# Kernel optimization log

Measured on AMD Instinct MI355X. Metric: run time of the kernel, lower is better.

Reference implementation:

```python
import jax, jax.numpy as jnp
import numpy as np

EPS = 1e-5

def _bn_bcn(x, g, b):
    # BatchNorm1d on [B, C, N], training mode: stats over (B, N) per channel
    m = x.mean(axis=(0, 2), keepdims=True)
    v = x.var(axis=(0, 2), keepdims=True)
    return g[None, :, None] * (x - m) * jax.lax.rsqrt(v + EPS) + b[None, :, None]

def _bn_bc(x, g, b):
    # BatchNorm1d on [B, C]
    m = x.mean(axis=0)
    v = x.var(axis=0)
    return g * (x - m) * jax.lax.rsqrt(v + EPS) + b

def _symmetric_orthogonalization(x9):
    # x9: [B, 9] -> [B, 3, 3] in SO(3)
    m = x9.reshape(-1, 3, 3)
    u, s, vt = jnp.linalg.svd(m, full_matrices=False)
    det = jnp.linalg.det(jnp.matmul(u, vt))[:, None, None]
    vt = jnp.concatenate([vt[:, :2, :], vt[:, 2:, :] * det], axis=1)
    return jnp.matmul(u, vt)

def setup_inputs() -> dict:
    key = jax.random.key(0)
    ks = jax.random.split(key, 24)
    B, N = 32, 2048
    def lin(k, out_c, in_c):
        return jax.random.normal(k, (out_c, in_c), jnp.float32) / np.sqrt(in_c)
    inp = {}
    inp['x'] = jax.random.normal(ks[0], (B, 3, N), jnp.float32)
    # conv1x1 weights (kernel size 1 -> per-point linear)
    inp['w1'] = lin(ks[1], 64, 3);    inp['b1'] = jnp.zeros((64,), jnp.float32)
    inp['g1'] = jnp.ones((64,), jnp.float32);   inp['be1'] = jnp.zeros((64,), jnp.float32)
    inp['w2'] = lin(ks[2], 128, 64);  inp['b2'] = jnp.zeros((128,), jnp.float32)
    inp['g2'] = jnp.ones((128,), jnp.float32);  inp['be2'] = jnp.zeros((128,), jnp.float32)
    inp['w3'] = lin(ks[3], 1024, 128); inp['b3'] = jnp.zeros((1024,), jnp.float32)
    inp['g3'] = jnp.ones((1024,), jnp.float32); inp['be3'] = jnp.zeros((1024,), jnp.float32)
    inp['wf1'] = lin(ks[4], 512, 1024); inp['bf1'] = jnp.zeros((512,), jnp.float32)
    inp['gf1'] = jnp.ones((512,), jnp.float32); inp['bef1'] = jnp.zeros((512,), jnp.float32)
    inp['wf2'] = lin(ks[5], 256, 512);  inp['bf2'] = jnp.zeros((256,), jnp.float32)
    inp['gf2'] = jnp.ones((256,), jnp.float32); inp['bef2'] = jnp.zeros((256,), jnp.float32)
    inp['wp'] = lin(ks[6], 12, 256);    inp['bp'] = jnp.zeros((12,), jnp.float32)
    return inp

def reference(x, w1, b1, g1, be1, w2, b2, g2, be2, w3, b3, g3, be3,
              wf1, bf1, gf1, bef1, wf2, bf2, gf2, bef2, wp, bp):
    B = x.shape[0]
    h = jax.nn.relu(_bn_bcn(jnp.einsum('bdn,od->bon', x, w1) + b1[None, :, None], g1, be1))
    h = jax.nn.relu(_bn_bcn(jnp.einsum('bdn,od->bon', h, w2) + b2[None, :, None], g2, be2))
    h = _bn_bcn(jnp.einsum('bdn,od->bon', h, w3) + b3[None, :, None], g3, be3)
    h = jnp.max(h, axis=2)                      # global max pool -> [B, 1024]
    h = jax.nn.relu(_bn_bc(h @ wf1.T + bf1, gf1, bef1))
    h = jax.nn.relu(_bn_bc(h @ wf2.T + bf2, gf2, bef2))
    p = h @ wp.T + bp                           # [B, 12]
    R = _symmetric_orthogonalization(p[:, :9])  # [B, 3, 3]
    t = p[:, 9:].reshape(-1, 3, 1)
    top = jnp.concatenate([R, t], axis=2)       # [B, 3, 4]
    pad = jnp.broadcast_to(jnp.array([0.0, 0.0, 0.0, 1.0], dtype=x.dtype), (B, 1, 4))
    return jnp.concatenate([top, pad], axis=1)  # [B, 4, 4]
```

## Files before the change

kernel.cpp:

```cpp
#include <hip/hip_runtime.h>


#define NPT 2048
#define C1 64
#define C2 128
#define EPSV 1e-5f

typedef __attribute__((ext_vector_type(8))) _Float16 half8;
typedef __attribute__((ext_vector_type(4))) float floatx4;

#define OFF_H1T   0
#define OFF_Y2H   2097152
#define OFF_H2T   6291456
#define OFF_Z     10485760
#define OFF_XS    (OFF_Z)
#define OFF_SUM2  (OFF_Z+16)
#define OFF_SQ2   (OFF_Z+144)
#define OFF_SUM3  (OFF_Z+272)
#define OFF_SQ3   (OFF_Z+1296)
#define OFF_F1R   (OFF_Z+2320)
#define OFF_F2R   (OFF_Z+18704)
#define ZN        26896
#define OFF_MX    (OFF_Z+26896)
#define OFF_MN    (OFF_MX+65536)
#define OFF_POOL  (OFF_MN+65536)
#define OFF_W3H   (OFF_POOL+32768)
#define OFF_W2H   (OFF_W3H+65536)
#define WS_FLOATS (OFF_W2H+4096)

static __device__ inline unsigned short f16r(float f) {
  _Float16 h = (_Float16)f;
  return __builtin_bit_cast(unsigned short, h);
}
static __device__ inline float h2f(unsigned short u) {
  return (float)__builtin_bit_cast(_Float16, u);
}
static __device__ inline int SW(int n, int cb) { return n ^ (((n >> 3) ^ cb) & 7); }

__global__ __launch_bounds__(256) void k_xstat(const float* __restrict__ x,
                                               float* __restrict__ xs)
{
  int idx4 = blockIdx.x * 256 + threadIdx.x;
  int n4 = idx4 & 511, b = idx4 >> 9;
  const float4* xr = (const float4*)(x + (size_t)b * 3 * NPT);
  float4 x0 = xr[n4], x1 = xr[512 + n4], x2 = xr[1024 + n4];
  float v[9];
  v[0] = x0.x + x0.y + x0.z + x0.w;
  v[1] = x1.x + x1.y + x1.z + x1.w;
  v[2] = x2.x + x2.y + x2.z + x2.w;
  v[3] = x0.x*x0.x + x0.y*x0.y + x0.z*x0.z + x0.w*x0.w;
  v[4] = x1.x*x1.x + x1.y*x1.y + x1.z*x1.z + x1.w*x1.w;
  v[5] = x2.x*x2.x + x2.y*x2.y + x2.z*x2.z + x2.w*x2.w;
  v[6] = x0.x*x1.x + x0.y*x1.y + x0.z*x1.z + x0.w*x1.w;
  v[7] = x0.x*x2.x + x0.y*x2.y + x0.z*x2.z + x0.w*x2.w;
  v[8] = x1.x*x2.x + x1.y*x2.y + x1.z*x2.z + x1.w*x2.w;
  #pragma unroll
  for (int k = 0; k < 9; ++k)
    for (int off = 32; off; off >>= 1) v[k] += __shfl_down(v[k], off);
  __shared__ float red[4][9];
  int lane = threadIdx.x & 63, wv = threadIdx.x >> 6;
  if (!lane)
    #pragma unroll
    for (int k = 0; k < 9; ++k) red[wv][k] = v[k];
  __syncthreads();
  if (threadIdx.x < 9)
    atomicAdd(&xs[threadIdx.x], red[0][threadIdx.x] + red[1][threadIdx.x] +
                                red[2][threadIdx.x] + red[3][threadIdx.x]);
}

__global__ __launch_bounds__(256) void k_cvt(const float* __restrict__ w3,
    const float* __restrict__ w2, unsigned short* __restrict__ w3h,
    unsigned short* __restrict__ w2h)
{
  int idx4 = blockIdx.x * 256 + threadIdx.x;
  const float4* src; ushort4* dst; int k;
  if (idx4 < 32768) { src = (const float4*)w3; dst = (ushort4*)w3h; k = idx4; }
  else               { src = (const float4*)w2; dst = (ushort4*)w2h; k = idx4 - 32768; }
  float4 v = src[k];
  ushort4 o;
  o.x = f16r(v.x); o.y = f16r(v.y); o.z = f16r(v.z); o.w = f16r(v.w);
  dst[k] = o;
}

__global__ __launch_bounds__(256) void k_conv1(const float* __restrict__ x,
    const float* __restrict__ w1, const float* __restrict__ b1,
    const float* __restrict__ g1, const float* __restrict__ be1,
    const float* __restrict__ xs, unsigned short* __restrict__ h1t)
{
  __shared__ float wc[64][4];
  int t = threadIdx.x;
  int bi = blockIdx.x;
  int b = bi >> 3, nt = bi & 7;
  if (t < 64) {
    float w0 = w1[t*3], w1_ = w1[t*3+1], w2_ = w1[t*3+2], bb = b1[t];
    const float invN = 1.f / 65536.f;
    float wsx = (w0*xs[0] + w1_*xs[1] + w2_*xs[2]) * invN;
    float mean = wsx + bb;
    float Ey2 = (w0*w0*xs[3] + w1_*w1_*xs[4] + w2_*w2_*xs[5]
               + 2.f*(w0*w1_*xs[6] + w0*w2_*xs[7] + w1_*w2_*xs[8])) * invN
               + 2.f*bb*wsx + bb*bb;
    float var = Ey2 - mean*mean;
    float a = g1[t] * rsqrtf(var + EPSV);
    wc[t][0] = a*w0; wc[t][1] = a*w1_; wc[t][2] = a*w2_;
    wc[t][3] = be1[t] + a*(bb - mean);
  }
  __syncthreads();
  int n = nt * 256 + t;
  const float* xb = x + (size_t)b * 3 * NPT + n;
  float x0 = xb[0], x1 = xb[NPT], x2 = xb[2*NPT];
  unsigned short* orow = h1t + ((size_t)b * NPT + n) * C1;
  #pragma unroll
  for (int i = 0; i < 8; ++i) {
    uint4 pk;
    unsigned* pd = (unsigned*)&pk;
    #pragma unroll
    for (int j = 0; j < 4; ++j) {
      int o = i*8 + j*2;
      float h0 = fmaxf(fmaf(wc[o][0], x0, fmaf(wc[o][1], x1, fmaf(wc[o][2], x2, wc[o][3]))), 0.f);
      float h1 = fmaxf(fmaf(wc[o+1][0], x0, fmaf(wc[o+1][1], x1, fmaf(wc[o+1][2], x2, wc[o+1][3]))), 0.f);
      pd[j] = (unsigned)f16r(h0) | ((unsigned)f16r(h1) << 16);
    }
    *(uint4*)(orow + i * 8) = pk;
  }
}

__global__ __launch_bounds__(256, 2) void k_conv2(const unsigned short* __restrict__ h1t,
    const unsigned short* __restrict__ w2h, const float* __restrict__ b2,
    unsigned short* __restrict__ y2h, float* __restrict__ sum2, float* __restrict__ sq2)
{
  __shared__ unsigned short w2s[8 * 128 * 8];
  __shared__ unsigned short h1s[8 * 64 * 8];
  __shared__ float sred[2][128][2];
  int t = threadIdx.x;
  int bi = blockIdx.x;
  int b = bi >> 5, ns = bi & 31;
  int n0 = ns * 64;
  int w = t >> 6, lane = t & 63;
  int ow = w & 1, nw = w >> 1;
  int quad = lane >> 4, l15 = lane & 15;

  for (int i = 0; i < 4; ++i) {
    int idx = i * 256 + t;
    int o = idx >> 3, cb = idx & 7;
    uint4 v = *(const uint4*)(w2h + o * 64 + cb * 8);
    int op = (o + cb) & 127;
    *(uint4*)&w2s[(cb * 128 + op) * 8] = v;
  }
  {
    int n = t & 63, cp = t >> 6;
    const unsigned short* src = h1t + ((size_t)b * NPT + n0 + n) * C1 + cp * 16;
    uint4 v0 = *(const uint4*)(src);
    uint4 v1 = *(const uint4*)(src + 8);
    *(uint4*)&h1s[((2*cp)   * 64 + SW(n, 2*cp))   * 8] = v0;
    *(uint4*)&h1s[((2*cp+1) * 64 + SW(n, 2*cp+1)) * 8] = v1;
  }
  __syncthreads();

  half8 af[4][2];
  #pragma unroll
  for (int ti = 0; ti < 4; ++ti)
    #pragma unroll
    for (int s = 0; s < 2; ++s) {
      int cb = s * 4 + quad;
      int o = ow * 64 + ti * 16 + l15;
      int op = (o + cb) & 127;
      af[ti][s] = *(const half8*)&w2s[(cb * 128 + op) * 8];
    }
  float breg[4][4];
  #pragma unroll
  for (int ti = 0; ti < 4; ++ti)
    #pragma unroll
    for (int r = 0; r < 4; ++r)
      breg[ti][r] = b2[ow * 64 + ti * 16 + quad * 4 + r];

  floatx4 acc[4][2];
  #pragma unroll
  for (int ti = 0; ti < 4; ++ti)
    #pragma unroll
    for (int nt = 0; nt < 2; ++nt) acc[ti][nt] = (floatx4){0.f, 0.f, 0.f, 0.f};
  #pragma unroll
  for (int s = 0; s < 2; ++s) {
    int cb = s * 4 + quad;
    half8 bf[2];
    #pragma unroll
    for (int nt = 0; nt < 2; ++nt) {
      int n = nw * 32 + nt * 16 + l15;
      bf[nt] = *(const half8*)&h1s[(cb * 64 + SW(n, cb)) * 8];
    }
    #pragma unroll
    for (int ti = 0; ti < 4; ++ti) {
      acc[ti][0] = __builtin_amdgcn_mfma_f32_16x16x32_f16(af[ti][s], bf[0], acc[ti][0], 0, 0, 0);
      acc[ti][1] = __builtin_amdgcn_mfma_f32_16x16x32_f16(af[ti][s], bf[1], acc[ti][1], 0, 0, 0);
    }
  }

  float sm[4][4], sq[4][4];
  #pragma unroll
  for (int ti = 0; ti < 4; ++ti)
    #pragma unroll
    for (int r = 0; r < 4; ++r) { sm[ti][r] = 0.f; sq[ti][r] = 0.f; }
  #pragma unroll
  for (int ti = 0; ti < 4; ++ti) {
    int o = ow * 64 + ti * 16 + quad * 4;
    #pragma unroll
    for (int nt = 0; nt < 2; ++nt) {
      int n = n0 + nw * 32 + nt * 16 + l15;
      #pragma unroll
      for (int r = 0; r < 4; ++r) {
        float val = acc[ti][nt][r] + breg[ti][r];
        y2h[(size_t)(b * C2 + o + r) * NPT + n] = f16r(val);
        sm[ti][r] += val;
        sq[ti][r] = fmaf(val, val, sq[ti][r]);
      }
    }
  }
  #pragma unroll
  for (int ti = 0; ti < 4; ++ti)
    #pragma unroll
    for (int r = 0; r < 4; ++r) {
      #pragma unroll
      for (int m = 1; m < 16; m <<= 1) {
        sm[ti][r] += __shfl_xor(sm[ti][r], m, 16);
        sq[ti][r] += __shfl_xor(sq[ti][r], m, 16);
      }
    }
  if (l15 == 0) {
    #pragma unroll
    for (int ti = 0; ti < 4; ++ti)
      #pragma unroll
      for (int r = 0; r < 4; ++r) {
        int oloc = ow * 64 + ti * 16 + quad * 4 + r;
        sred[nw][oloc][0] = sm[ti][r];
        sred[nw][oloc][1] = sq[ti][r];
      }
  }
  __syncthreads();
  if (t < 128) {
    atomicAdd(&sum2[t], sred[0][t][0] + sred[1][t][0]);
    atomicAdd(&sq2[t],  sred[0][t][1] + sred[1][t][1]);
  }
}

__global__ __launch_bounds__(256) void k_bnrelu2(const unsigned short* __restrict__ y2h,
    const float* __restrict__ sum2, const float* __restrict__ sq2,
    const float* __restrict__ g2, const float* __restrict__ be2,
    unsigned short* __restrict__ h2t)
{
  __shared__ float bn[128][2];
  int t = threadIdx.x;
  int bi = blockIdx.x;
  int b = bi >> 5, nt = bi & 31;
  int n0 = nt * 64;
  if (t < 128) {
    float m = sum2[t] * (1.f / 65536.f);
    float v = fmaf(-m, m, sq2[t] * (1.f / 65536.f));
    float a = g2[t] * rsqrtf(v + EPSV);
    bn[t][0] = a; bn[t][1] = fmaf(-a, m, be2[t]);
  }
  __syncthreads();
  int coct = t & 15, ng = t >> 4;
  int c0 = coct * 8, n = n0 + ng * 4;
  float h[8][4];
  #pragma unroll
  for (int i = 0; i < 8; ++i) {
    ushort4 u = *(const ushort4*)(y2h + (size_t)(b * C2 + c0 + i) * NPT + n);
    float a = bn[c0 + i][0], s = bn[c0 + i][1];
    h[i][0] = fmaxf(fmaf(a, h2f(u.x), s), 0.f);
    h[i][1] = fmaxf(fmaf(a, h2f(u.y), s), 0.f);
    h[i][2] = fmaxf(fmaf(a, h2f(u.z), s), 0.f);
    h[i][3] = fmaxf(fmaf(a, h2f(u.w), s), 0.f);
  }
  #pragma unroll
  for (int j = 0; j < 4; ++j) {
    uint4 pk;
    pk.x = (unsigned)f16r(h[0][j]) | ((unsigned)f16r(h[1][j]) << 16);
    pk.y = (unsigned)f16r(h[2][j]) | ((unsigned)f16r(h[3][j]) << 16);
    pk.z = (unsigned)f16r(h[4][j]) | ((unsigned)f16r(h[5][j]) << 16);
    pk.w = (unsigned)f16r(h[6][j]) | ((unsigned)f16r(h[7][j]) << 16);
    *(uint4*)(h2t + ((size_t)b * NPT + n + j) * C2 + c0) = pk;
  }
}

__global__ __launch_bounds__(256, 2) void k_conv3(const unsigned short* __restrict__ h2t,
    const unsigned short* __restrict__ w3h, const float* __restrict__ b3,
    float* __restrict__ mxb, float* __restrict__ mnb,
    float* __restrict__ sum3, float* __restrict__ sq3)
{
  __shared__ unsigned short w3s[16 * 128 * 8];
  __shared__ unsigned short h2s[16 * 64 * 8];
  __shared__ float sred[2][128][4];
  int t = threadIdx.x;
  int bi = blockIdx.x;
  int ot_blk = bi >> 6;
  int b  = (bi >> 1) & 31;
  int ns = bi & 1;
  int o0 = ot_blk * 128;
  int n_base = ns * 1024;
  int w = t >> 6, lane = t & 63;
  int ow = w & 1, nw = w >> 1;
  int quad = lane >> 4, l15 = lane & 15;

  for (int i = 0; i < 8; ++i) {
    int idx = i * 256 + t;
    int o = idx >> 4, cb = idx & 15;
    uint4 v = *(const uint4*)(w3h + (size_t)(o0 + o) * 128 + cb * 8);
    int op = (o + cb) & 127;
    *(uint4*)&w3s[(cb * 128 + op) * 8] = v;
  }
  __syncthreads();

  half8 af[4][4];
  #pragma unroll
  for (int ti = 0; ti < 4; ++ti)
    #pragma unroll
    for (int s = 0; s < 4; ++s) {
      int cb = s * 4 + quad;
      int o = ow * 64 + ti * 16 + l15;
      int op = (o + cb) & 127;
      af[ti][s] = *(const half8*)&w3s[(cb * 128 + op) * 8];
    }

  float breg[4][4], mx[4][4], mn[4][4], sm[4][4], sq[4][4];
  #pragma unroll
  for (int ti = 0; ti < 4; ++ti)
    #pragma unroll
    for (int r = 0; r < 4; ++r) {
      breg[ti][r] = b3[o0 + ow * 64 + ti * 16 + quad * 4 + r];
      mx[ti][r] = -3.4e38f; mn[ti][r] = 3.4e38f; sm[ti][r] = 0.f; sq[ti][r] = 0.f;
    }

  int sn = t & 63, cq = t >> 6;
  for (int nc = 0; nc < 16; ++nc) {
    int n0 = n_base + nc * 64;
    __syncthreads();
    {
      const unsigned short* src = h2t + ((size_t)b * NPT + n0 + sn) * C2 + cq * 32;
      uint4 v0 = *(const uint4*)(src);
      uint4 v1 = *(const uint4*)(src + 8);
      uint4 v2 = *(const uint4*)(src + 16);
      uint4 v3 = *(const uint4*)(src + 24);
      int cb0 = cq * 4;
      *(uint4*)&h2s[((cb0 + 0) * 64 + SW(sn, cb0 + 0)) * 8] = v0;
      *(uint4*)&h2s[((cb0 + 1) * 64 + SW(sn, cb0 + 1)) * 8] = v1;
      *(uint4*)&h2s[((cb0 + 2) * 64 + SW(sn, cb0 + 2)) * 8] = v2;
      *(uint4*)&h2s[((cb0 + 3) * 64 + SW(sn, cb0 + 3)) * 8] = v3;
    }
    __syncthreads();

    floatx4 acc[4][2];
    #pragma unroll
    for (int ti = 0; ti < 4; ++ti)
      #pragma unroll
      for (int nt = 0; nt < 2; ++nt) acc[ti][nt] = (floatx4){0.f, 0.f, 0.f, 0.f};
    #pragma unroll
    for (int s = 0; s < 4; ++s) {
      int cb = s * 4 + quad;
      half8 bf[2];
      #pragma unroll
      for (int nt = 0; nt < 2; ++nt) {
        int n = nw * 32 + nt * 16 + l15;
        bf[nt] = *(const half8*)&h2s[(cb * 64 + SW(n, cb)) * 8];
      }
      #pragma unroll
      for (int ti = 0; ti < 4; ++ti) {
        acc[ti][0] = __builtin_amdgcn_mfma_f32_16x16x32_f16(af[ti][s], bf[0], acc[ti][0], 0, 0, 0);
        acc[ti][1] = __builtin_amdgcn_mfma_f32_16x16x32_f16(af[ti][s], bf[1], acc[ti][1], 0, 0, 0);
      }
    }
    #pragma unroll
    for (int ti = 0; ti < 4; ++ti)
      #pragma unroll
      for (int nt = 0; nt < 2; ++nt)
        #pragma unroll
        for (int r = 0; r < 4; ++r) {
          float v = acc[ti][nt][r] + breg[ti][r];
          mx[ti][r] = fmaxf(mx[ti][r], v);
          mn[ti][r] = fminf(mn[ti][r], v);
          sm[ti][r] += v;
          sq[ti][r] = fmaf(v, v, sq[ti][r]);
        }
  }

  #pragma unroll
  for (int ti = 0; ti < 4; ++ti)
    #pragma unroll
    for (int r = 0; r < 4; ++r) {
      #pragma unroll
      for (int m = 1; m < 16; m <<= 1) {
        mx[ti][r] = fmaxf(mx[ti][r], __shfl_xor(mx[ti][r], m, 16));
        mn[ti][r] = fminf(mn[ti][r], __shfl_xor(mn[ti][r], m, 16));
        sm[ti][r] += __shfl_xor(sm[ti][r], m, 16);
        sq[ti][r] += __shfl_xor(sq[ti][r], m, 16);
      }
    }
  if (l15 == 0) {
    #pragma unroll
    for (int ti = 0; ti < 4; ++ti)
      #pragma unroll
      for (int r = 0; r < 4; ++r) {
        int oloc = ow * 64 + ti * 16 + quad * 4 + r;
        sred[nw][oloc][0] = mx[ti][r];
        sred[nw][oloc][1] = mn[ti][r];
        sred[nw][oloc][2] = sm[ti][r];
        sred[nw][oloc][3] = sq[ti][r];
      }
  }
  __syncthreads();
  if (t < 128) {
    int o = o0 + t;
    mxb[ns * 32768 + b * 1024 + o] = fmaxf(sred[0][t][0], sred[1][t][0]);
    mnb[ns * 32768 + b * 1024 + o] = fminf(sred[0][t][1], sred[1][t][1]);
    atomicAdd(&sum3[o], sred[0][t][2] + sred[1][t][2]);
    atomicAdd(&sq3[o],  sred[0][t][3] + sred[1][t][3]);
  }
}

__global__ __launch_bounds__(256) void k_pooled(const float* __restrict__ sum3,
    const float* __restrict__ sq3, const float* __restrict__ g3,
    const float* __restrict__ be3, const float* __restrict__ mxb,
    const float* __restrict__ mnb, float* __restrict__ pool)
{
  int idx4 = blockIdx.x * 256 + threadIdx.x;
  int c4 = idx4 & 255;
  float4 S = ((const float4*)sum3)[c4];
  float4 Q = ((const float4*)sq3)[c4];
  float4 G = ((const float4*)g3)[c4];
  float4 Be = ((const float4*)be3)[c4];
  float4 a, s;
  const float inv = 1.f / 65536.f;
  #define MK(c) { float m = S.c * inv; float v = fmaf(-m, m, Q.c * inv); \
                  a.c = G.c * rsqrtf(v + EPSV); s.c = fmaf(-a.c, m, Be.c); }
  MK(x) MK(y) MK(z) MK(w)
  #undef MK
  float4 mx = ((const float4*)mxb)[idx4];
  float4 mn = ((const float4*)mnb)[idx4];
  {
    float4 mxs = ((const float4*)mxb)[idx4 + 8192];
    float4 mns = ((const float4*)mnb)[idx4 + 8192];
    mx.x = fmaxf(mx.x, mxs.x); mx.y = fmaxf(mx.y, mxs.y);
    mx.z = fmaxf(mx.z, mxs.z); mx.w = fmaxf(mx.w, mxs.w);
    mn.x = fminf(mn.x, mns.x); mn.y = fminf(mn.y, mns.y);
    mn.z = fminf(mn.z, mns.z); mn.w = fminf(mn.w, mns.w);
  }
  float4 r;
  r.x = fmaf(a.x, (a.x >= 0.f ? mx.x : mn.x), s.x);
  r.y = fmaf(a.y, (a.y >= 0.f ? mx.y : mn.y), s.y);
  r.z = fmaf(a.z, (a.z >= 0.f ? mx.z : mn.z), s.z);
  r.w = fmaf(a.w, (a.w >= 0.f ? mx.w : mn.w), s.w);
  ((float4*)pool)[idx4] = r;
}

__global__ __launch_bounds__(256) void k_fc1(const float* __restrict__ pool,
    const float* __restrict__ wf1, const float* __restrict__ bf1,
    float* __restrict__ f1r)
{
  __shared__ float ins[32 * 128];
  int t = threadIdx.x;
  int f0 = blockIdx.x * 32;
  int k0 = blockIdx.y * 128;
  #pragma unroll
  for (int i = 0; i < 4; ++i) {
    int idx = i * 256 + t;
    int b = idx >> 5, k4 = idx & 31;
    *(float4*)&ins[b * 128 + k4 * 4] = *(const float4*)(pool + (size_t)b * 1024 + k0 + k4 * 4);
  }
  __syncthreads();
  int f = t & 31, bq = t >> 5;
  int bl = bq * 4;
  const float4* wr = (const float4*)(wf1 + (size_t)(f0 + f) * 1024 + k0);
  float acc0 = 0.f, acc1 = 0.f, acc2 = 0.f, acc3 = 0.f;
  #pragma unroll 4
  for (int k4 = 0; k4 < 32; ++k4) {
    float4 wv = wr[k4];
    float4 i0 = *(const float4*)&ins[(bl + 0) * 128 + k4 * 4];
    float4 i1 = *(const float4*)&ins[(bl + 1) * 128 + k4 * 4];
    float4 i2 = *(const float4*)&ins[(bl + 2) * 128 + k4 * 4];
    float4 i3 = *(const float4*)&ins[(bl + 3) * 128 + k4 * 4];
    acc0 = fmaf(wv.x, i0.x, fmaf(wv.y, i0.y, fmaf(wv.z, i0.z, fmaf(wv.w, i0.w, acc0))));
    acc1 = fmaf(wv.x, i1.x, fmaf(wv.y, i1.y, fmaf(wv.z, i1.z, fmaf(wv.w, i1.w, acc1))));
    acc2 = fmaf(wv.x, i2.x, fmaf(wv.y, i2.y, fmaf(wv.z, i2.z, fmaf(wv.w, i2.w, acc2))));
    acc3 = fmaf(wv.x, i3.x, fmaf(wv.y, i3.y, fmaf(wv.z, i3.z, fmaf(wv.w, i3.w, acc3))));
  }
  float bs = (blockIdx.y == 0) ? bf1[f0 + f] : 0.f;
  atomicAdd(&f1r[(size_t)(bl + 0) * 512 + f0 + f], acc0 + bs);
  atomicAdd(&f1r[(size_t)(bl + 1) * 512 + f0 + f], acc1 + bs);
  atomicAdd(&f1r[(size_t)(bl + 2) * 512 + f0 + f], acc2 + bs);
  atomicAdd(&f1r[(size_t)(bl + 3) * 512 + f0 + f], acc3 + bs);
}

__global__ __launch_bounds__(256) void k_fc2(const float* __restrict__ f1r,
    const float* __restrict__ wf2, const float* __restrict__ bf2,
    const float* __restrict__ gf1, const float* __restrict__ bef1,
    float* __restrict__ f2r)
{
  __shared__ float ins[32 * 64];
  __shared__ float bnA[64], bnS[64];
  int t = threadIdx.x;
  int f0 = blockIdx.x * 32;
  int k0 = blockIdx.y * 64;
  #pragma unroll
  for (int i = 0; i < 2; ++i) {
    int idx = i * 256 + t;
    int b = idx >> 4, k4 = idx & 15;
    *(float4*)&ins[b * 64 + k4 * 4] = *(const float4*)(f1r + (size_t)b * 512 + k0 + k4 * 4);
  }
  __syncthreads();
  if (t < 64) {
    float s = 0.f, q = 0.f;
    #pragma unroll
    for (int b = 0; b < 32; ++b) {
      float x = ins[b * 64 + t];
      s += x; q = fmaf(x, x, q);
    }
    float m = s * (1.f / 32.f);
    float v = fmaf(-m, m, q * (1.f / 32.f));
    float a = gf1[k0 + t] * rsqrtf(v + EPSV);
    bnA[t] = a; bnS[t] = fmaf(-a, m, bef1[k0 + t]);
  }
  __syncthreads();
  #pragma unroll
  for (int i = 0; i < 2; ++i) {
    int idx = i * 256 + t;
    int b = idx >> 4, k4 = idx & 15;
    float4 v = *(const float4*)&ins[b * 64 + k4 * 4];
    v.x = fmaxf(fmaf(bnA[k4*4+0], v.x, bnS[k4*4+0]), 0.f);
    v.y = fmaxf(fmaf(bnA[k4*4+1], v.y, bnS[k4*4+1]), 0.f);
    v.z = fmaxf(fmaf(bnA[k4*4+2], v.z, bnS[k4*4+2]), 0.f);
    v.w = fmaxf(fmaf(bnA[k4*4+3], v.w, bnS[k4*4+3]), 0.f);
    *(float4*)&ins[b * 64 + k4 * 4] = v;
  }
  __syncthreads();
  int f = t & 31, bq = t >> 5;
  int bl = bq * 4;
  const float4* wr = (const float4*)(wf2 + (size_t)(f0 + f) * 512 + k0);
  float acc0 = 0.f, acc1 = 0.f, acc2 = 0.f, acc3 = 0.f;
  #pragma unroll 4
  for (int k4 = 0; k4 < 16; ++k4) {
    float4 wv = wr[k4];
    float4 i0 = *(const float4*)&ins[(bl + 0) * 64 + k4 * 4];
    float4 i1 = *(const float4*)&ins[(bl + 1) * 64 + k4 * 4];
    float4 i2 = *(const float4*)&ins[(bl + 2) * 64 + k4 * 4];
    float4 i3 = *(const float4*)&ins[(bl + 3) * 64 + k4 * 4];
    acc0 = fmaf(wv.x, i0.x, fmaf(wv.y, i0.y, fmaf(wv.z, i0.z, fmaf(wv.w, i0.w, acc0))));
    acc1 = fmaf(wv.x, i1.x, fmaf(wv.y, i1.y, fmaf(wv.z, i1.z, fmaf(wv.w, i1.w, acc1))));
    acc2 = fmaf(wv.x, i2.x, fmaf(wv.y, i2.y, fmaf(wv.z, i2.z, fmaf(wv.w, i2.w, acc2))));
    acc3 = fmaf(wv.x, i3.x, fmaf(wv.y, i3.y, fmaf(wv.w, i3.w, fmaf(wv.z, i3.z, acc3))));
  }
  float bs = (blockIdx.y == 0) ? bf2[f0 + f] : 0.f;
  atomicAdd(&f2r[(size_t)(bl + 0) * 256 + f0 + f], acc0 + bs);
  atomicAdd(&f2r[(size_t)(bl + 1) * 256 + f0 + f], acc1 + bs);
  atomicAdd(&f2r[(size_t)(bl + 2) * 256 + f0 + f], acc2 + bs);
  atomicAdd(&f2r[(size_t)(bl + 3) * 256 + f0 + f], acc3 + bs);
}

__global__ __launch_bounds__(384) void k_head(const float* __restrict__ f2r,
    const float* __restrict__ gf2, const float* __restrict__ bef2,
    const float* __restrict__ wp, const float* __restrict__ bp,
    float* __restrict__ out)
{
  __shared__ float pS[32 * 12];
  __shared__ float bnf[256][2];
  int t = threadIdx.x;
  if (t < 256) {
    float s = 0.f, q = 0.f;
    #pragma unroll
    for (int b = 0; b < 32; ++b) {
      float x = f2r[b * 256 + t];
      s += x; q = fmaf(x, x, q);
    }
    float m = s * (1.f / 32.f);
    float v = fmaf(-m, m, q * (1.f / 32.f));
    float a = gf2[t] * rsqrtf(v + EPSV);
    bnf[t][0] = a; bnf[t][1] = fmaf(-a, m, bef2[t]);
  }
  __syncthreads();
  {
    int b = t / 12, j = t % 12;
    const float* w = wp + j * 256;
    const float* fr = f2r + b * 256;
    float acc = bp[j];
    #pragma unroll 8
    for (int c = 0; c < 256; ++c) {
      float h = fmaxf(fmaf(bnf[c][0], fr[c], bnf[c][1]), 0.f);
      acc = fmaf(w[c], h, acc);
    }
    pS[t] = acc;
  }
  __syncthreads();
  if (t < 32) {
    const float* p = &pS[t * 12];
    float m00=p[0],m01=p[1],m02=p[2],m10=p[3],m11=p[4],m12=p[5],m20=p[6],m21=p[7],m22=p[8];
    float P[4][4];
    P[0][0]=m00+m11+m22; P[0][1]=m21-m12;     P[0][2]=m02-m20;     P[0][3]=m10-m01;
    P[1][1]=m00-m11-m22; P[1][2]=m01+m10;     P[1][3]=m02+m20;
    P[2][2]=m11-m00-m22; P[2][3]=m12+m21;
    P[3][3]=m22-m00-m11;
    P[1][0]=P[0][1]; P[2][0]=P[0][2]; P[3][0]=P[0][3];
    P[2][1]=P[1][2]; P[3][1]=P[1][3]; P[3][2]=P[2][3];
    float fn = sqrtf(m00*m00+m01*m01+m02*m02+m10*m10+m11*m11+m12*m12+m20*m20+m21*m21+m22*m22);
    float inv = 1.f / (2.f * fn + 1e-30f);
    #pragma unroll
    for (int i = 0; i < 4; ++i)
      #pragma unroll
      for (int j = 0; j < 4; ++j) P[i][j] *= inv;
    P[0][0] += 1.f; P[1][1] += 1.f; P[2][2] += 1.f; P[3][3] += 1.f;
    for (int it = 0; it < 16; ++it) {
      float Q[4][4];
      #pragma unroll
      for (int i = 0; i < 4; ++i)
        #pragma unroll
        for (int j = 0; j < 4; ++j)
          Q[i][j] = P[i][0]*P[0][j] + P[i][1]*P[1][j] + P[i][2]*P[2][j] + P[i][3]*P[3][j];
      float mxa = 0.f;
      #pragma unroll
      for (int i = 0; i < 4; ++i)
        #pragma unroll
        for (int j = 0; j < 4; ++j) mxa = fmaxf(mxa, fabsf(Q[i][j]));
      float r = 1.f / mxa;
      #pragma unroll
      for (int i = 0; i < 4; ++i)
        #pragma unroll
        for (int j = 0; j < 4; ++j) P[i][j] = Q[i][j] * r;
    }
    float bestn = -1.f; int bj = 0;
    #pragma unroll
    for (int j = 0; j < 4; ++j) {
      float nn = P[0][j]*P[0][j] + P[1][j]*P[1][j] + P[2][j]*P[2][j] + P[3][j]*P[3][j];
      if (nn > bestn) { bestn = nn; bj = j; }
    }
    float qw = P[0][bj], qx = P[1][bj], qy = P[2][bj], qz = P[3][bj];
    float qn = rsqrtf(qw*qw + qx*qx + qy*qy + qz*qz);
    qw *= qn; qx *= qn; qy *= qn; qz *= qn;
    float* ob = out + t * 16;
    ob[0]  = 1.f - 2.f*(qy*qy + qz*qz);
    ob[1]  = 2.f*(qx*qy - qw*qz);
    ob[2]  = 2.f*(qx*qz + qw*qy);
    ob[3]  = p[9];
    ob[4]  = 2.f*(qx*qy + qw*qz);
    ob[5]  = 1.f - 2.f*(qx*qx + qz*qz);
    ob[6]  = 2.f*(qy*qz - qw*qx);
    ob[7]  = p[10];
    ob[8]  = 2.f*(qx*qz - qw*qy);
    ob[9]  = 2.f*(qy*qz + qw*qx);
    ob[10] = 1.f - 2.f*(qx*qx + qy*qy);
    ob[11] = p[11];
    ob[12] = 0.f; ob[13] = 0.f; ob[14] = 0.f; ob[15] = 1.f;
  }
}

extern "C" void kernel_launch(void* const* d_in, const int* in_sizes, int n_in,
                              void* d_out, int out_size, void* d_ws, size_t ws_size,
                              hipStream_t stream)
{
  (void)in_sizes; (void)n_in; (void)out_size;
  if (ws_size < (size_t)WS_FLOATS * sizeof(float)) return;
  const float* x   = (const float*)d_in[0];
  const float* w1  = (const float*)d_in[1];
  const float* b1  = (const float*)d_in[2];
  const float* g1  = (const float*)d_in[3];
  const float* be1 = (const float*)d_in[4];
  const float* w2  = (const float*)d_in[5];
  const float* b2  = (const float*)d_in[6];
  const float* g2  = (const float*)d_in[7];
  const float* be2 = (const float*)d_in[8];
  const float* w3  = (const float*)d_in[9];
  const float* b3  = (const float*)d_in[10];
  const float* g3  = (const float*)d_in[11];
  const float* be3 = (const float*)d_in[12];
  const float* wf1 = (const float*)d_in[13];
  const float* bf1 = (const float*)d_in[14];
  const float* gf1 = (const float*)d_in[15];
  const float* bef1= (const float*)d_in[16];
  const float* wf2 = (const float*)d_in[17];
  const float* bf2 = (const float*)d_in[18];
  const float* gf2 = (const float*)d_in[19];
  const float* bef2= (const float*)d_in[20];
  const float* wp  = (const float*)d_in[21];
  const float* bp  = (const float*)d_in[22];
  float* ws  = (float*)d_ws;
  float* out = (float*)d_out;
  unsigned short* h1t = (unsigned short*)(ws + OFF_H1T);
  unsigned short* y2h = (unsigned short*)(ws + OFF_Y2H);
  unsigned short* h2t = (unsigned short*)(ws + OFF_H2T);
  unsigned short* w3h = (unsigned short*)(ws + OFF_W3H);
  unsigned short* w2h = (unsigned short*)(ws + OFF_W2H);

  hipMemsetAsync((void*)(ws + OFF_Z), 0, ZN * sizeof(float), stream);
  k_cvt<<<136, 256, 0, stream>>>(w3, w2, w3h, w2h);
  k_xstat<<<64, 256, 0, stream>>>(x, ws + OFF_XS);
  k_conv1<<<256, 256, 0, stream>>>(x, w1, b1, g1, be1, ws + OFF_XS, h1t);
  k_conv2<<<1024, 256, 0, stream>>>(h1t, w2h, b2, y2h, ws + OFF_SUM2, ws + OFF_SQ2);
  k_bnrelu2<<<1024, 256, 0, stream>>>(y2h, ws + OFF_SUM2, ws + OFF_SQ2, g2, be2, h2t);
  k_conv3<<<512, 256, 0, stream>>>(h2t, w3h, b3, ws + OFF_MX, ws + OFF_MN,
                                   ws + OFF_SUM3, ws + OFF_SQ3);
  k_pooled<<<32, 256, 0, stream>>>(ws + OFF_SUM3, ws + OFF_SQ3, g3, be3,
                                   ws + OFF_MX, ws + OFF_MN, ws + OFF_POOL);
  k_fc1<<<dim3(16, 8), 256, 0, stream>>>(ws + OFF_POOL, wf1, bf1, ws + OFF_F1R);
  k_fc2<<<dim3(8, 8), 256, 0, stream>>>(ws + OFF_F1R, wf2, bf2, gf1, bef1, ws + OFF_F2R);
  k_head<<<1, 384, 0, stream>>>(ws + OFF_F2R, gf2, bef2, wp, bp, out);
}
```

Baseline: 221.4 us.

## Fuse conv1 into conv2, merge prep kernels, fold pooling BN into fc1

```diff
diff --git a/kernel.cpp b/kernel.cpp
--- a/kernel.cpp
+++ b/kernel.cpp
@@ -9,10 +9,9 @@
 typedef __attribute__((ext_vector_type(8))) _Float16 half8;
 typedef __attribute__((ext_vector_type(4))) float floatx4;
 
-#define OFF_H1T   0
-#define OFF_Y2H   2097152
-#define OFF_H2T   6291456
-#define OFF_Z     10485760
+#define OFF_Y2T   0
+#define OFF_H2T   4194304
+#define OFF_Z     8388608
 #define OFF_XS    (OFF_Z)
 #define OFF_SUM2  (OFF_Z+16)
 #define OFF_SQ2   (OFF_Z+144)
@@ -23,8 +22,7 @@
 #define ZN        26896
 #define OFF_MX    (OFF_Z+26896)
 #define OFF_MN    (OFF_MX+65536)
-#define OFF_POOL  (OFF_MN+65536)
-#define OFF_W3H   (OFF_POOL+32768)
+#define OFF_W3H   (OFF_MN+65536)
 #define OFF_W2H   (OFF_W3H+65536)
 #define WS_FLOATS (OFF_W2H+4096)
 
@@ -37,10 +35,25 @@
 }
 static __device__ inline int SW(int n, int cb) { return n ^ (((n >> 3) ^ cb) & 7); }
 
-__global__ __launch_bounds__(256) void k_xstat(const float* __restrict__ x,
-                                               float* __restrict__ xs)
-{
-  int idx4 = blockIdx.x * 256 + threadIdx.x;
+__global__ __launch_bounds__(256) void k_prep(const float* __restrict__ w3,
+    const float* __restrict__ w2, unsigned short* __restrict__ w3h,
+    unsigned short* __restrict__ w2h, const float* __restrict__ x,
+    float* __restrict__ xs)
+{
+  int bi = blockIdx.x;
+  int t = threadIdx.x;
+  if (bi < 136) {
+    int idx4 = bi * 256 + t;
+    const float4* src; ushort4* dst; int k;
+    if (idx4 < 32768) { src = (const float4*)w3; dst = (ushort4*)w3h; k = idx4; }
+    else               { src = (const float4*)w2; dst = (ushort4*)w2h; k = idx4 - 32768; }
+    float4 v = src[k];
+    ushort4 o;
+    o.x = f16r(v.x); o.y = f16r(v.y); o.z = f16r(v.z); o.w = f16r(v.w);
+    dst[k] = o;
+    return;
+  }
+  int idx4 = (bi - 136) * 256 + t;
   int n4 = idx4 & 511, b = idx4 >> 9;
   const float4* xr = (const float4*)(x + (size_t)b * 3 * NPT);
   float4 x0 = xr[n4], x1 = xr[512 + n4], x2 = xr[1024 + n4];
@@ -58,39 +71,34 @@
   for (int k = 0; k < 9; ++k)
     for (int off = 32; off; off >>= 1) v[k] += __shfl_down(v[k], off);
   __shared__ float red[4][9];
-  int lane = threadIdx.x & 63, wv = threadIdx.x >> 6;
+  int lane = t & 63, wv = t >> 6;
   if (!lane)
     #pragma unroll
     for (int k = 0; k < 9; ++k) red[wv][k] = v[k];
   __syncthreads();
-  if (threadIdx.x < 9)
-    atomicAdd(&xs[threadIdx.x], red[0][threadIdx.x] + red[1][threadIdx.x] +
-                                red[2][threadIdx.x] + red[3][threadIdx.x]);
-}
-
-__global__ __launch_bounds__(256) void k_cvt(const float* __restrict__ w3,
-    const float* __restrict__ w2, unsigned short* __restrict__ w3h,
-    unsigned short* __restrict__ w2h)
-{
-  int idx4 = blockIdx.x * 256 + threadIdx.x;
-  const float4* src; ushort4* dst; int k;
-  if (idx4 < 32768) { src = (const float4*)w3; dst = (ushort4*)w3h; k = idx4; }
-  else               { src = (const float4*)w2; dst = (ushort4*)w2h; k = idx4 - 32768; }
-  float4 v = src[k];
-  ushort4 o;
-  o.x = f16r(v.x); o.y = f16r(v.y); o.z = f16r(v.z); o.w = f16r(v.w);
-  dst[k] = o;
-}
-
-__global__ __launch_bounds__(256) void k_conv1(const float* __restrict__ x,
+  if (t < 9)
+    atomicAdd(&xs[t], red[0][t] + red[1][t] + red[2][t] + red[3][t]);
+}
+
+__global__ __launch_bounds__(256, 4) void k_conv12(const float* __restrict__ x,
     const float* __restrict__ w1, const float* __restrict__ b1,
     const float* __restrict__ g1, const float* __restrict__ be1,
-    const float* __restrict__ xs, unsigned short* __restrict__ h1t)
-{
+    const float* __restrict__ xs,
+    const unsigned short* __restrict__ w2h, const float* __restrict__ b2,
+    unsigned short* __restrict__ y2t, float* __restrict__ sum2, float* __restrict__ sq2)
+{
+  __shared__ unsigned short w2s[8 * 128 * 8];
+  __shared__ unsigned short h1s[8 * 64 * 8];
   __shared__ float wc[64][4];
+  __shared__ float sred[2][128][2];
   int t = threadIdx.x;
   int bi = blockIdx.x;
-  int b = bi >> 3, nt = bi & 7;
+  int b = bi >> 5, ns = bi & 31;
+  int n0 = ns * 64;
+  int w = t >> 6, lane = t & 63;
+  int ow = w & 1, nw = w >> 1;
+  int quad = lane >> 4, l15 = lane & 15;
+
   if (t < 64) {
     float w0 = w1[t*3], w1_ = w1[t*3+1], w2_ = w1[t*3+2], bb = b1[t];
     const float invN = 1.f / 65536.f;
@@ -104,41 +112,6 @@
     wc[t][0] = a*w0; wc[t][1] = a*w1_; wc[t][2] = a*w2_;
     wc[t][3] = be1[t] + a*(bb - mean);
   }
-  __syncthreads();
-  int n = nt * 256 + t;
-  const float* xb = x + (size_t)b * 3 * NPT + n;
-  float x0 = xb[0], x1 = xb[NPT], x2 = xb[2*NPT];
-  unsigned short* orow = h1t + ((size_t)b * NPT + n) * C1;
-  #pragma unroll
-  for (int i = 0; i < 8; ++i) {
-    uint4 pk;
-    unsigned* pd = (unsigned*)&pk;
-    #pragma unroll
-    for (int j = 0; j < 4; ++j) {
-      int o = i*8 + j*2;
-      float h0 = fmaxf(fmaf(wc[o][0], x0, fmaf(wc[o][1], x1, fmaf(wc[o][2], x2, wc[o][3]))), 0.f);
-      float h1 = fmaxf(fmaf(wc[o+1][0], x0, fmaf(wc[o+1][1], x1, fmaf(wc[o+1][2], x2, wc[o+1][3]))), 0.f);
-      pd[j] = (unsigned)f16r(h0) | ((unsigned)f16r(h1) << 16);
-    }
-    *(uint4*)(orow + i * 8) = pk;
-  }
-}
-
-__global__ __launch_bounds__(256, 2) void k_conv2(const unsigned short* __restrict__ h1t,
-    const unsigned short* __restrict__ w2h, const float* __restrict__ b2,
-    unsigned short* __restrict__ y2h, float* __restrict__ sum2, float* __restrict__ sq2)
-{
-  __shared__ unsigned short w2s[8 * 128 * 8];
-  __shared__ unsigned short h1s[8 * 64 * 8];
-  __shared__ float sred[2][128][2];
-  int t = threadIdx.x;
-  int bi = blockIdx.x;
-  int b = bi >> 5, ns = bi & 31;
-  int n0 = ns * 64;
-  int w = t >> 6, lane = t & 63;
-  int ow = w & 1, nw = w >> 1;
-  int quad = lane >> 4, l15 = lane & 15;
-
   for (int i = 0; i < 4; ++i) {
     int idx = i * 256 + t;
     int o = idx >> 3, cb = idx & 7;
@@ -146,13 +119,30 @@
     int op = (o + cb) & 127;
     *(uint4*)&w2s[(cb * 128 + op) * 8] = v;
   }
+  __syncthreads();
+
   {
-    int n = t & 63, cp = t >> 6;
-    const unsigned short* src = h1t + ((size_t)b * NPT + n0 + n) * C1 + cp * 16;
-    uint4 v0 = *(const uint4*)(src);
-    uint4 v1 = *(const uint4*)(src + 8);
-    *(uint4*)&h1s[((2*cp)   * 64 + SW(n, 2*cp))   * 8] = v0;
-    *(uint4*)&h1s[((2*cp+1) * 64 + SW(n, 2*cp+1)) * 8] = v1;
+    int cg = t >> 5, ng = t & 31;
+    int c0 = cg * 8, nn = ng * 2;
+    const float* xb = x + (size_t)b * 3 * NPT + n0 + nn;
+    float2 xv0 = *(const float2*)(xb);
+    float2 xv1 = *(const float2*)(xb + NPT);
+    float2 xv2 = *(const float2*)(xb + 2 * NPT);
+    uint4 p0, p1;
+    unsigned* a0 = (unsigned*)&p0;
+    unsigned* a1 = (unsigned*)&p1;
+    #pragma unroll
+    for (int j = 0; j < 4; ++j) {
+      int c = c0 + j * 2;
+      float hA0 = fmaxf(fmaf(wc[c][0], xv0.x, fmaf(wc[c][1], xv1.x, fmaf(wc[c][2], xv2.x, wc[c][3]))), 0.f);
+      float hA1 = fmaxf(fmaf(wc[c][0], xv0.y, fmaf(wc[c][1], xv1.y, fmaf(wc[c][2], xv2.y, wc[c][3]))), 0.f);
+      float hB0 = fmaxf(fmaf(wc[c+1][0], xv0.x, fmaf(wc[c+1][1], xv1.x, fmaf(wc[c+1][2], xv2.x, wc[c+1][3]))), 0.f);
+      float hB1 = fmaxf(fmaf(wc[c+1][0], xv0.y, fmaf(wc[c+1][1], xv1.y, fmaf(wc[c+1][2], xv2.y, wc[c+1][3]))), 0.f);
+      a0[j] = (unsigned)f16r(hA0) | ((unsigned)f16r(hB0) << 16);
+      a1[j] = (unsigned)f16r(hA1) | ((unsigned)f16r(hB1) << 16);
+    }
+    *(uint4*)&h1s[(cg * 64 + SW(nn, cg)) * 8] = p0;
+    *(uint4*)&h1s[(cg * 64 + SW(nn + 1, cg)) * 8] = p1;
   }
   __syncthreads();
 
@@ -205,13 +195,17 @@
     #pragma unroll
     for (int nt = 0; nt < 2; ++nt) {
       int n = n0 + nw * 32 + nt * 16 + l15;
-      #pragma unroll
-      for (int r = 0; r < 4; ++r) {
-        float val = acc[ti][nt][r] + breg[ti][r];
-        y2h[(size_t)(b * C2 + o + r) * NPT + n] = f16r(val);
-        sm[ti][r] += val;
-        sq[ti][r] = fmaf(val, val, sq[ti][r]);
-      }
+      float v0 = acc[ti][nt][0] + breg[ti][0];
+      float v1 = acc[ti][nt][1] + breg[ti][1];
+      float v2 = acc[ti][nt][2] + breg[ti][2];
+      float v3 = acc[ti][nt][3] + breg[ti][3];
+      ushort4 st;
+      st.x = f16r(v0); st.y = f16r(v1); st.z = f16r(v2); st.w = f16r(v3);
+      *(ushort4*)(y2t + ((size_t)b * NPT + n) * C2 + o) = st;
+      sm[ti][0] += v0; sq[ti][0] = fmaf(v0, v0, sq[ti][0]);
+      sm[ti][1] += v1; sq[ti][1] = fmaf(v1, v1, sq[ti][1]);
+      sm[ti][2] += v2; sq[ti][2] = fmaf(v2, v2, sq[ti][2]);
+      sm[ti][3] += v3; sq[ti][3] = fmaf(v3, v3, sq[ti][3]);
     }
   }
   #pragma unroll
@@ -241,16 +235,13 @@
   }
 }
 
-__global__ __launch_bounds__(256) void k_bnrelu2(const unsigned short* __restrict__ y2h,
+__global__ __launch_bounds__(256) void k_bnrelu2(const unsigned short* __restrict__ y2t,
     const float* __restrict__ sum2, const float* __restrict__ sq2,
     const float* __restrict__ g2, const float* __restrict__ be2,
     unsigned short* __restrict__ h2t)
 {
   __shared__ float bn[128][2];
   int t = threadIdx.x;
-  int bi = blockIdx.x;
-  int b = bi >> 5, nt = bi & 31;
-  int n0 = nt * 64;
   if (t < 128) {
     float m = sum2[t] * (1.f / 65536.f);
     float v = fmaf(-m, m, sq2[t] * (1.f / 65536.f));
@@ -258,26 +249,27 @@
     bn[t][0] = a; bn[t][1] = fmaf(-a, m, be2[t]);
   }
   __syncthreads();
-  int coct = t & 15, ng = t >> 4;
-  int c0 = coct * 8, n = n0 + ng * 4;
-  float h[8][4];
-  #pragma unroll
-  for (int i = 0; i < 8; ++i) {
-    ushort4 u = *(const ushort4*)(y2h + (size_t)(b * C2 + c0 + i) * NPT + n);
-    float a = bn[c0 + i][0], s = bn[c0 + i][1];
-    h[i][0] = fmaxf(fmaf(a, h2f(u.x), s), 0.f);
-    h[i][1] = fmaxf(fmaf(a, h2f(u.y), s), 0.f);
-    h[i][2] = fmaxf(fmaf(a, h2f(u.z), s), 0.f);
-    h[i][3] = fmaxf(fmaf(a, h2f(u.w), s), 0.f);
-  }
-  #pragma unroll
-  for (int j = 0; j < 4; ++j) {
+  size_t base = ((size_t)blockIdx.x * 256 + t) * 32;
+  int c0 = (int)(base & 127);
+  #pragma unroll
+  for (int k = 0; k < 4; ++k) {
+    ushort4 u0 = *(const ushort4*)(y2t + base + k * 8);
+    ushort4 u1 = *(const ushort4*)(y2t + base + k * 8 + 4);
+    int c = c0 + k * 8;
+    float h0 = fmaxf(fmaf(bn[c+0][0], h2f(u0.x), bn[c+0][1]), 0.f);
+    float h1 = fmaxf(fmaf(bn[c+1][0], h2f(u0.y), bn[c+1][1]), 0.f);
+    float h2 = fmaxf(fmaf(bn[c+2][0], h2f(u0.z), bn[c+2][1]), 0.f);
+    float h3 = fmaxf(fmaf(bn[c+3][0], h2f(u0.w), bn[c+3][1]), 0.f);
+    float h4 = fmaxf(fmaf(bn[c+4][0], h2f(u1.x), bn[c+4][1]), 0.f);
+    float h5 = fmaxf(fmaf(bn[c+5][0], h2f(u1.y), bn[c+5][1]), 0.f);
+    float h6 = fmaxf(fmaf(bn[c+6][0], h2f(u1.z), bn[c+6][1]), 0.f);
+    float h7 = fmaxf(fmaf(bn[c+7][0], h2f(u1.w), bn[c+7][1]), 0.f);
     uint4 pk;
-    pk.x = (unsigned)f16r(h[0][j]) | ((unsigned)f16r(h[1][j]) << 16);
-    pk.y = (unsigned)f16r(h[2][j]) | ((unsigned)f16r(h[3][j]) << 16);
-    pk.z = (unsigned)f16r(h[4][j]) | ((unsigned)f16r(h[5][j]) << 16);
-    pk.w = (unsigned)f16r(h[6][j]) | ((unsigned)f16r(h[7][j]) << 16);
-    *(uint4*)(h2t + ((size_t)b * NPT + n + j) * C2 + c0) = pk;
+    pk.x = (unsigned)f16r(h0) | ((unsigned)f16r(h1) << 16);
+    pk.y = (unsigned)f16r(h2) | ((unsigned)f16r(h3) << 16);
+    pk.z = (unsigned)f16r(h4) | ((unsigned)f16r(h5) << 16);
+    pk.w = (unsigned)f16r(h6) | ((unsigned)f16r(h7) << 16);
+    *(uint4*)(h2t + base + k * 8) = pk;
   }
 }
 
@@ -320,12 +312,11 @@
       af[ti][s] = *(const half8*)&w3s[(cb * 128 + op) * 8];
     }
 
-  float breg[4][4], mx[4][4], mn[4][4], sm[4][4], sq[4][4];
+  float mx[4][4], mn[4][4], sm[4][4], sq[4][4];
   #pragma unroll
   for (int ti = 0; ti < 4; ++ti)
     #pragma unroll
     for (int r = 0; r < 4; ++r) {
-      breg[ti][r] = b3[o0 + ow * 64 + ti * 16 + quad * 4 + r];
       mx[ti][r] = -3.4e38f; mn[ti][r] = 3.4e38f; sm[ti][r] = 0.f; sq[ti][r] = 0.f;
     }
 
@@ -373,7 +364,7 @@
       for (int nt = 0; nt < 2; ++nt)
         #pragma unroll
         for (int r = 0; r < 4; ++r) {
-          float v = acc[ti][nt][r] + breg[ti][r];
+          float v = acc[ti][nt][r];
           mx[ti][r] = fmaxf(mx[ti][r], v);
           mn[ti][r] = fminf(mn[ti][r], v);
           sm[ti][r] += v;
@@ -408,61 +399,53 @@
   __syncthreads();
   if (t < 128) {
     int o = o0 + t;
-    mxb[ns * 32768 + b * 1024 + o] = fmaxf(sred[0][t][0], sred[1][t][0]);
-    mnb[ns * 32768 + b * 1024 + o] = fminf(sred[0][t][1], sred[1][t][1]);
-    atomicAdd(&sum3[o], sred[0][t][2] + sred[1][t][2]);
-    atomicAdd(&sq3[o],  sred[0][t][3] + sred[1][t][3]);
-  }
-}
-
-__global__ __launch_bounds__(256) void k_pooled(const float* __restrict__ sum3,
+    float bo = b3[o];
+    float fmx = fmaxf(sred[0][t][0], sred[1][t][0]) + bo;
+    float fmn = fminf(sred[0][t][1], sred[1][t][1]) + bo;
+    float smr = sred[0][t][2] + sred[1][t][2];
+    float sqr = sred[0][t][3] + sred[1][t][3];
+    mxb[ns * 32768 + b * 1024 + o] = fmx;
+    mnb[ns * 32768 + b * 1024 + o] = fmn;
+    atomicAdd(&sum3[o], fmaf(1024.f, bo, smr));
+    atomicAdd(&sq3[o],  fmaf(1024.f * bo, bo, fmaf(2.f * bo, smr, sqr)));
+  }
+}
+
+__global__ __launch_bounds__(256) void k_fc1(const float* __restrict__ mxb,
+    const float* __restrict__ mnb, const float* __restrict__ sum3,
     const float* __restrict__ sq3, const float* __restrict__ g3,
-    const float* __restrict__ be3, const float* __restrict__ mxb,
-    const float* __restrict__ mnb, float* __restrict__ pool)
-{
-  int idx4 = blockIdx.x * 256 + threadIdx.x;
-  int c4 = idx4 & 255;
-  float4 S = ((const float4*)sum3)[c4];
-  float4 Q = ((const float4*)sq3)[c4];
-  float4 G = ((const float4*)g3)[c4];
-  float4 Be = ((const float4*)be3)[c4];
-  float4 a, s;
-  const float inv = 1.f / 65536.f;
-  #define MK(c) { float m = S.c * inv; float v = fmaf(-m, m, Q.c * inv); \
-                  a.c = G.c * rsqrtf(v + EPSV); s.c = fmaf(-a.c, m, Be.c); }
-  MK(x) MK(y) MK(z) MK(w)
-  #undef MK
-  float4 mx = ((const float4*)mxb)[idx4];
-  float4 mn = ((const float4*)mnb)[idx4];
-  {
-    float4 mxs = ((const float4*)mxb)[idx4 + 8192];
-    float4 mns = ((const float4*)mnb)[idx4 + 8192];
-    mx.x = fmaxf(mx.x, mxs.x); mx.y = fmaxf(mx.y, mxs.y);
-    mx.z = fmaxf(mx.z, mxs.z); mx.w = fmaxf(mx.w, mxs.w);
-    mn.x = fminf(mn.x, mns.x); mn.y = fminf(mn.y, mns.y);
-    mn.z = fminf(mn.z, mns.z); mn.w = fminf(mn.w, mns.w);
-  }
-  float4 r;
-  r.x = fmaf(a.x, (a.x >= 0.f ? mx.x : mn.x), s.x);
-  r.y = fmaf(a.y, (a.y >= 0.f ? mx.y : mn.y), s.y);
-  r.z = fmaf(a.z, (a.z >= 0.f ? mx.z : mn.z), s.z);
-  r.w = fmaf(a.w, (a.w >= 0.f ? mx.w : mn.w), s.w);
-  ((float4*)pool)[idx4] = r;
-}
-
-__global__ __launch_bounds__(256) void k_fc1(const float* __restrict__ pool,
-    const float* __restrict__ wf1, const float* __restrict__ bf1,
-    float* __restrict__ f1r)
+    const float* __restrict__ be3, const float* __restrict__ wf1,
+    const float* __restrict__ bf1, float* __restrict__ f1r)
 {
   __shared__ float ins[32 * 128];
+  __shared__ float bnA[128], bnS[128];
   int t = threadIdx.x;
   int f0 = blockIdx.x * 32;
   int k0 = blockIdx.y * 128;
+  if (t < 128) {
+    int c = k0 + t;
+    float m = sum3[c] * (1.f / 65536.f);
+    float v = fmaf(-m, m, sq3[c] * (1.f / 65536.f));
+    float a = g3[c] * rsqrtf(v + EPSV);
+    bnA[t] = a; bnS[t] = fmaf(-a, m, be3[c]);
+  }
+  __syncthreads();
   #pragma unroll
   for (int i = 0; i < 4; ++i) {
     int idx = i * 256 + t;
     int b = idx >> 5, k4 = idx & 31;
-    *(float4*)&ins[b * 128 + k4 * 4] = *(const float4*)(pool + (size_t)b * 1024 + k0 + k4 * 4);
+    float4 mxv = *(const float4*)(mxb + (size_t)b * 1024 + k0 + k4 * 4);
+    float4 mx1 = *(const float4*)(mxb + 32768 + (size_t)b * 1024 + k0 + k4 * 4);
+    float4 mnv = *(const float4*)(mnb + (size_t)b * 1024 + k0 + k4 * 4);
+    float4 mn1 = *(const float4*)(mnb + 32768 + (size_t)b * 1024 + k0 + k4 * 4);
+    float4 a = *(const float4*)&bnA[k4 * 4];
+    float4 s = *(const float4*)&bnS[k4 * 4];
+    float4 r;
+    r.x = fmaf(a.x, (a.x >= 0.f ? fmaxf(mxv.x, mx1.x) : fminf(mnv.x, mn1.x)), s.x);
+    r.y = fmaf(a.y, (a.y >= 0.f ? fmaxf(mxv.y, mx1.y) : fminf(mnv.y, mn1.y)), s.y);
+    r.z = fmaf(a.z, (a.z >= 0.f ? fmaxf(mxv.z, mx1.z) : fminf(mnv.z, mn1.z)), s.z);
+    r.w = fmaf(a.w, (a.w >= 0.f ? fmaxf(mxv.w, mx1.w) : fminf(mnv.w, mn1.w)), s.w);
+    *(float4*)&ins[b * 128 + k4 * 4] = r;
   }
   __syncthreads();
   int f = t & 31, bq = t >> 5;
@@ -509,8 +492,8 @@
     float s = 0.f, q = 0.f;
     #pragma unroll
     for (int b = 0; b < 32; ++b) {
-      float x = ins[b * 64 + t];
-      s += x; q = fmaf(x, x, q);
+      float xx = ins[b * 64 + t];
+      s += xx; q = fmaf(xx, xx, q);
     }
     float m = s * (1.f / 32.f);
     float v = fmaf(-m, m, q * (1.f / 32.f));
@@ -544,7 +527,7 @@
     acc0 = fmaf(wv.x, i0.x, fmaf(wv.y, i0.y, fmaf(wv.z, i0.z, fmaf(wv.w, i0.w, acc0))));
     acc1 = fmaf(wv.x, i1.x, fmaf(wv.y, i1.y, fmaf(wv.z, i1.z, fmaf(wv.w, i1.w, acc1))));
     acc2 = fmaf(wv.x, i2.x, fmaf(wv.y, i2.y, fmaf(wv.z, i2.z, fmaf(wv.w, i2.w, acc2))));
-    acc3 = fmaf(wv.x, i3.x, fmaf(wv.y, i3.y, fmaf(wv.w, i3.w, fmaf(wv.z, i3.z, acc3))));
+    acc3 = fmaf(wv.x, i3.x, fmaf(wv.y, i3.y, fmaf(wv.z, i3.z, fmaf(wv.w, i3.w, acc3))));
   }
   float bs = (blockIdx.y == 0) ? bf2[f0 + f] : 0.f;
   atomicAdd(&f2r[(size_t)(bl + 0) * 256 + f0 + f], acc0 + bs);
@@ -565,8 +548,8 @@
     float s = 0.f, q = 0.f;
     #pragma unroll
     for (int b = 0; b < 32; ++b) {
-      float x = f2r[b * 256 + t];
-      s += x; q = fmaf(x, x, q);
+      float xx = f2r[b * 256 + t];
+      s += xx; q = fmaf(xx, xx, q);
     }
     float m = s * (1.f / 32.f);
     float v = fmaf(-m, m, q * (1.f / 32.f));
@@ -679,23 +662,20 @@
   const float* bp  = (const float*)d_in[22];
   float* ws  = (float*)d_ws;
   float* out = (float*)d_out;
-  unsigned short* h1t = (unsigned short*)(ws + OFF_H1T);
-  unsigned short* y2h = (unsigned short*)(ws + OFF_Y2H);
+  unsigned short* y2t = (unsigned short*)(ws + OFF_Y2T);
   unsigned short* h2t = (unsigned short*)(ws + OFF_H2T);
   unsigned short* w3h = (unsigned short*)(ws + OFF_W3H);
   unsigned short* w2h = (unsigned short*)(ws + OFF_W2H);
 
   hipMemsetAsync((void*)(ws + OFF_Z), 0, ZN * sizeof(float), stream);
-  k_cvt<<<136, 256, 0, stream>>>(w3, w2, w3h, w2h);
-  k_xstat<<<64, 256, 0, stream>>>(x, ws + OFF_XS);
-  k_conv1<<<256, 256, 0, stream>>>(x, w1, b1, g1, be1, ws + OFF_XS, h1t);
-  k_conv2<<<1024, 256, 0, stream>>>(h1t, w2h, b2, y2h, ws + OFF_SUM2, ws + OFF_SQ2);
-  k_bnrelu2<<<1024, 256, 0, stream>>>(y2h, ws + OFF_SUM2, ws + OFF_SQ2, g2, be2, h2t);
+  k_prep<<<200, 256, 0, stream>>>(w3, w2, w3h, w2h, x, ws + OFF_XS);
+  k_conv12<<<1024, 256, 0, stream>>>(x, w1, b1, g1, be1, ws + OFF_XS,
+                                     w2h, b2, y2t, ws + OFF_SUM2, ws + OFF_SQ2);
+  k_bnrelu2<<<1024, 256, 0, stream>>>(y2t, ws + OFF_SUM2, ws + OFF_SQ2, g2, be2, h2t);
   k_conv3<<<512, 256, 0, stream>>>(h2t, w3h, b3, ws + OFF_MX, ws + OFF_MN,
                                    ws + OFF_SUM3, ws + OFF_SQ3);
-  k_pooled<<<32, 256, 0, stream>>>(ws + OFF_SUM3, ws + OFF_SQ3, g3, be3,
-                                   ws + OFF_MX, ws + OFF_MN, ws + OFF_POOL);
-  k_fc1<<<dim3(16, 8), 256, 0, stream>>>(ws + OFF_POOL, wf1, bf1, ws + OFF_F1R);
+  k_fc1<<<dim3(16, 8), 256, 0, stream>>>(ws + OFF_MX, ws + OFF_MN, ws + OFF_SUM3,
+                                         ws + OFF_SQ3, g3, be3, wf1, bf1, ws + OFF_F1R);
   k_fc2<<<dim3(8, 8), 256, 0, stream>>>(ws + OFF_F1R, wf2, bf2, gf1, bef1, ws + OFF_F2R);
   k_head<<<1, 384, 0, stream>>>(ws + OFF_F2R, gf2, bef2, wp, bp, out);
 }
```

Result: faster. 211.1 us (-4.7%).
